# Optimization experiments

Measured on AMD Instinct MI355X. Metric: run time of the kernel, lower is better.

## Reference

```python
import jax, jax.numpy as jnp
import numpy as np

IN_CH, OUT_CH, HEAD, QK_DIM, V_DIM = 256, 256, 8, 512, 512


def setup_inputs() -> dict:
    key = jax.random.key(0)
    ks = jax.random.split(key, 5)
    B, H, W = 16, 32, 32
    x = jax.random.normal(ks[0], (B, IN_CH, H, W), dtype=jnp.float32)
    # 1x1 conv weights stored as [out_ch, in_ch]
    qkv_out = 2 * QK_DIM + V_DIM
    qkv_w = jax.random.normal(ks[1], (qkv_out, IN_CH), dtype=jnp.float32) * (IN_CH ** -0.5)
    qkv_b = jax.random.normal(ks[2], (qkv_out,), dtype=jnp.float32) * 0.02
    proj_w = jax.random.normal(ks[3], (OUT_CH, V_DIM), dtype=jnp.float32) * (V_DIM ** -0.5)
    proj_b = jax.random.normal(ks[4], (OUT_CH,), dtype=jnp.float32) * 0.02
    return {"x": x, "qkv_w": qkv_w, "qkv_b": qkv_b, "proj_w": proj_w, "proj_b": proj_b}


def reference(x, qkv_w, qkv_b, proj_w, proj_b):
    B, C, H, W = x.shape
    N = H * W
    dh = QK_DIM // HEAD
    dv = V_DIM // HEAD
    scale = dh ** -0.5
    # 1x1 conv == channel GEMM
    qkv = jnp.einsum('bchw,oc->bohw', x, qkv_w) + qkv_b[None, :, None, None]
    q, k, v = jnp.split(qkv, [QK_DIM, 2 * QK_DIM], axis=1)
    # [B, ch, H, W] -> [B, head, N, head_dim]
    def to_heads(t, d):
        return t.reshape(B, HEAD, d, N).transpose(0, 1, 3, 2)
    q = to_heads(q, dh)
    k = to_heads(k, dh)
    v = to_heads(v, dv)
    mask = jnp.tril(jnp.ones((N, N), dtype=bool))  # [N, N]
    scores = jnp.einsum('bhnd,bhmd->bhnm', q, k) * scale
    scores = jnp.where(mask, scores, -jnp.inf)
    attn = jax.nn.softmax(scores, axis=-1)
    attn = jnp.where(mask, attn, 0.0)
    out = jnp.einsum('bhnm,bhmd->bhnd', attn, v)  # [B, head, N, dv]
    out = out.transpose(0, 1, 3, 2).reshape(B, V_DIM, H, W)
    out = jnp.einsum('bvhw,ov->bohw', out, proj_w) + proj_b[None, :, None, None]
    return out
```

## Files before the change

kernel.cpp:

```cpp
#include <hip/hip_runtime.h>
#include <math.h>

static constexpr int Bsz = 16;
static constexpr int Np  = 1024;
static constexpr int Cin = 256;

typedef __attribute__((ext_vector_type(8))) short short8;
typedef __attribute__((ext_vector_type(4))) float f4;

#if defined(__has_builtin)
#if __has_builtin(__builtin_amdgcn_exp2f)
#define EXP2(x) __builtin_amdgcn_exp2f(x)
#else
#define EXP2(x) exp2f(x)
#endif
#else
#define EXP2(x) exp2f(x)
#endif

#define QSCALE 0.18033688011112f

__device__ __forceinline__ unsigned short f2b(float f) {
    union { float fp; unsigned int u; } v; v.fp = f;
    unsigned int r = v.u + 0x7fffu + ((v.u >> 16) & 1u);
    return (unsigned short)(r >> 16);
}

__global__ __launch_bounds__(256)
void cast_xw(const float* __restrict__ x, const float* __restrict__ qw,
             const float* __restrict__ pw, ushort* __restrict__ xb,
             ushort* __restrict__ qwb, ushort* __restrict__ pwb)
{
    const int t = threadIdx.x;
    if (blockIdx.y < 4) {
        __shared__ ushort T[64][72];
        const int n0 = blockIdx.x * 64, c0 = blockIdx.y * 64, b = blockIdx.z;
        {
            const int c_l = t >> 2, ns = (t & 3) * 16;
            const float* src = &x[((b * Cin + c0 + c_l) << 10) + n0 + ns];
#pragma unroll
            for (int i = 0; i < 4; ++i) {
                const float4 v = *(const float4*)(src + 4 * i);
                T[ns + 4 * i + 0][c_l] = f2b(v.x);
                T[ns + 4 * i + 1][c_l] = f2b(v.y);
                T[ns + 4 * i + 2][c_l] = f2b(v.z);
                T[ns + 4 * i + 3][c_l] = f2b(v.w);
            }
        }
        __syncthreads();
        {
            const int n_l = t >> 2, cs = (t & 3) * 16;
            ushort* dst = &xb[((b << 10) + n0 + n_l) * Cin + c0 + cs];
            *(uint4*)dst       = *(const uint4*)&T[n_l][cs];
            *(uint4*)(dst + 8) = *(const uint4*)&T[n_l][cs + 8];
        }
    } else {
        const int nq4 = (1536 * Cin) / 4;
        const int base = ((blockIdx.z * 16 + blockIdx.x) * 256 + t) * 2;
#pragma unroll
        for (int g = 0; g < 2; ++g) {
            const int j = base + g;
            const float* src; ushort* dst; int jj;
            if (j < nq4) { src = qw; dst = qwb; jj = j; }
            else         { src = pw; dst = pwb; jj = j - nq4; }
            const float4 v = *(const float4*)(src + 4 * jj);
            ushort4 u; u.x = f2b(v.x); u.y = f2b(v.y); u.z = f2b(v.z); u.w = f2b(v.w);
            *(ushort4*)(dst + 4 * jj) = u;
        }
    }
}

__global__ __launch_bounds__(256)
void qkv_gemm(const ushort* __restrict__ xb, const ushort* __restrict__ wb,
              const float* __restrict__ bias,
              ushort* __restrict__ qb, ushort* __restrict__ kb, ushort* __restrict__ vb)
{
    __shared__ ushort lds[18432];
    ushort* As = lds;
    ushort* Bs = lds + 9216;

    const int t = threadIdx.x;
    const int w = t >> 6, lane = t & 63, quad = lane >> 4, ln = lane & 15;
    const int n0 = blockIdx.x * 128;
    const int o0 = blockIdx.y * 128;
    const int b  = blockIdx.z;
    const int ow = (w & 1) * 64, nw = (w >> 1) * 64;
    const bool vpath = (o0 >= 1024);

    f4 acc[4][4];
#pragma unroll
    for (int i = 0; i < 4; ++i)
#pragma unroll
        for (int j = 0; j < 4; ++j) acc[i][j] = (f4){0.f, 0.f, 0.f, 0.f};

    const int rr = t >> 2, cc = (t & 3) * 16;
    for (int k0 = 0; k0 < Cin; k0 += 64) {
        __syncthreads();
#pragma unroll
        for (int p = 0; p < 2; ++p) {
            const int row = rr + p * 64;
            const ushort* sa = &wb[(o0 + row) * Cin + k0 + cc];
            *(uint4*)&As[row * 72 + cc]     = *(const uint4*)sa;
            *(uint4*)&As[row * 72 + cc + 8] = *(const uint4*)(sa + 8);
            const ushort* sb = &xb[((b << 10) + n0 + row) * Cin + k0 + cc];
            *(uint4*)&Bs[row * 72 + cc]     = *(const uint4*)sb;
            *(uint4*)&Bs[row * 72 + cc + 8] = *(const uint4*)(sb + 8);
        }
        __syncthreads();
#pragma unroll
        for (int sub = 0; sub < 2; ++sub) {
            short8 af[4], bf[4];
#pragma unroll
            for (int ot = 0; ot < 4; ++ot)
                af[ot] = *(const short8*)&As[(ow + ot * 16 + ln) * 72 + sub * 32 + quad * 8];
#pragma unroll
            for (int nt = 0; nt < 4; ++nt)
                bf[nt] = *(const short8*)&Bs[(nw + nt * 16 + ln) * 72 + sub * 32 + quad * 8];
            if (!vpath) {
#pragma unroll
                for (int ot = 0; ot < 4; ++ot)
#pragma unroll
                    for (int nt = 0; nt < 4; ++nt)
                        acc[ot][nt] = __builtin_amdgcn_mfma_f32_16x16x32_bf16(
                            af[ot], bf[nt], acc[ot][nt], 0, 0, 0);
            } else {
#pragma unroll
                for (int nt = 0; nt < 4; ++nt)
#pragma unroll
                    for (int ot = 0; ot < 4; ++ot)
                        acc[nt][ot] = __builtin_amdgcn_mfma_f32_16x16x32_bf16(
                            bf[nt], af[ot], acc[nt][ot], 0, 0, 0);
            }
        }
    }

    __syncthreads();
    if (!vpath) {
        ushort* Ct = lds;
        const float sc = (o0 < 512) ? QSCALE : 1.0f;
#pragma unroll
        for (int ot = 0; ot < 4; ++ot) {
            float bs[4];
#pragma unroll
            for (int rg = 0; rg < 4; ++rg)
                bs[rg] = bias[o0 + ow + ot * 16 + quad * 4 + rg];
#pragma unroll
            for (int nt = 0; nt < 4; ++nt) {
                ushort4 u;
                u.x = f2b((acc[ot][nt][0] + bs[0]) * sc);
                u.y = f2b((acc[ot][nt][1] + bs[1]) * sc);
                u.z = f2b((acc[ot][nt][2] + bs[2]) * sc);
                u.w = f2b((acc[ot][nt][3] + bs[3]) * sc);
                *(ushort4*)&Ct[(nw + nt * 16 + ln) * 136 + ow + ot * 16 + quad * 4] = u;
            }
        }
        __syncthreads();
        ushort* dst; int obase;
        if (o0 < 512) { dst = qb; obase = o0; }
        else          { dst = kb; obase = o0 - 512; }
        const int rn = t >> 1, hf = t & 1;
        const int bh = b * 8 + (obase >> 6) + hf;
        ushort* drow = &dst[(bh * Np + n0 + rn) << 6];
        const ushort* srow = &Ct[rn * 136 + hf * 64];
#pragma unroll
        for (int s = 0; s < 8; ++s)
            *(uint4*)(drow + s * 8) = *(const uint4*)(srow + s * 8);
    } else {
        ushort* Ct = lds;
#pragma unroll
        for (int ot = 0; ot < 4; ++ot) {
            const float bo = bias[o0 + ow + ot * 16 + ln];
#pragma unroll
            for (int nt = 0; nt < 4; ++nt) {
                ushort4 u;
                u.x = f2b(acc[nt][ot][0] + bo);
                u.y = f2b(acc[nt][ot][1] + bo);
                u.z = f2b(acc[nt][ot][2] + bo);
                u.w = f2b(acc[nt][ot][3] + bo);
                *(ushort4*)&Ct[(ow + ot * 16 + ln) * 136 + nw + nt * 16 + quad * 4] = u;
            }
        }
        __syncthreads();
        const int o_l = t >> 1, nh = (t & 1) * 64;
        const int bh = b * 8 + ((o0 - 1024) >> 6) + (o_l >> 6);
        ushort* drow = &vb[((size_t)bh << 16) + ((o_l & 63) << 10) + n0 + nh];
        const ushort* srow = &Ct[o_l * 136 + nh];
#pragma unroll
        for (int s = 0; s < 8; ++s)
            *(uint4*)(drow + s * 8) = *(const uint4*)(srow + s * 8);
    }
}

__global__ __launch_bounds__(256, 4)
void attn(const ushort* __restrict__ qb, const ushort* __restrict__ kb,
          const ushort* __restrict__ vt, ushort* __restrict__ ob)
{
    __shared__ ushort Qs[64 * 72];
    __shared__ ushort Ks[64 * 72];
    __shared__ ushort Vt[64 * 72];
    __shared__ ushort Ps[64 * 72];

    const int t    = threadIdx.x;
    const int w    = t >> 6;
    const int lane = t & 63;
    const int quad = lane >> 4;
    const int ln   = lane & 15;
    const int bh   = blockIdx.x & 127;
    const int qt   = 15 - (blockIdx.x >> 7);
    const int q0   = qt * 64;

    {
        const int r = t & 63, seg = t >> 6;
        const ushort* src = &qb[((bh * Np + q0 + r) << 6) + seg * 16];
        *(uint4*)&Qs[r * 72 + seg * 16]     = *(const uint4*)src;
        *(uint4*)&Qs[r * 72 + seg * 16 + 8] = *(const uint4*)(src + 8);
    }
    __syncthreads();

    const short8 qa0 = *(const short8*)&Qs[(w * 16 + ln) * 72 + quad * 8];
    const short8 qa1 = *(const short8*)&Qs[(w * 16 + ln) * 72 + 32 + quad * 8];

    f4 o_[4];
#pragma unroll
    for (int nt = 0; nt < 4; ++nt) o_[nt] = (f4){0.f, 0.f, 0.f, 0.f};
    float mrun = -INFINITY, lrun = 0.f;

    for (int kt = 0; kt <= qt; ++kt) {
        __syncthreads();
        {
            const int r = t & 63, seg = t >> 6;
            const ushort* sk = &kb[((bh * Np + kt * 64 + r) << 6) + seg * 16];
            *(uint4*)&Ks[r * 72 + seg * 16]     = *(const uint4*)sk;
            *(uint4*)&Ks[r * 72 + seg * 16 + 8] = *(const uint4*)(sk + 8);
            const int dd = t >> 2, c = (t & 3) * 16;
            const ushort* sv = &vt[((size_t)bh << 16) + (dd << 10) + kt * 64 + c];
            *(uint4*)&Vt[dd * 72 + c]     = *(const uint4*)sv;
            *(uint4*)&Vt[dd * 72 + c + 8] = *(const uint4*)(sv + 8);
        }
        __syncthreads();

        const bool diag = (kt == qt);

        f4 st[4];
#pragma unroll
        for (int mt = 0; mt < 4; ++mt) st[mt] = (f4){0.f, 0.f, 0.f, 0.f};
#pragma unroll
        for (int mt = 0; mt < 4; ++mt) {
            if (diag && mt > w) continue;
            const short8 ka0 = *(const short8*)&Ks[(mt * 16 + ln) * 72 + quad * 8];
            const short8 ka1 = *(const short8*)&Ks[(mt * 16 + ln) * 72 + 32 + quad * 8];
            st[mt] = __builtin_amdgcn_mfma_f32_16x16x32_bf16(ka0, qa0, st[mt], 0, 0, 0);
            st[mt] = __builtin_amdgcn_mfma_f32_16x16x32_bf16(ka1, qa1, st[mt], 0, 0, 0);
        }

        if (diag) {
            const int qrow = w * 16 + ln;
#pragma unroll
            for (int mt = 0; mt < 4; ++mt)
#pragma unroll
                for (int rg = 0; rg < 4; ++rg)
                    if (mt * 16 + quad * 4 + rg > qrow) st[mt][rg] = -INFINITY;
        }

        float mx = -INFINITY;
#pragma unroll
        for (int mt = 0; mt < 4; ++mt)
#pragma unroll
            for (int rg = 0; rg < 4; ++rg) mx = fmaxf(mx, st[mt][rg]);
        mx = fmaxf(mx, __shfl_xor(mx, 16));
        mx = fmaxf(mx, __shfl_xor(mx, 32));

        const float mn = fmaxf(mrun, mx);
        const float al = EXP2(mrun - mn);
        mrun = mn;

        float rs = 0.f;
        const int prow = (w * 16 + ln) * 72;
#pragma unroll
        for (int mt = 0; mt < 4; ++mt) {
            float p0 = EXP2(st[mt][0] - mn), p1 = EXP2(st[mt][1] - mn);
            float p2 = EXP2(st[mt][2] - mn), p3 = EXP2(st[mt][3] - mn);
            rs += (p0 + p1) + (p2 + p3);
            ushort4 u; u.x = f2b(p0); u.y = f2b(p1); u.z = f2b(p2); u.w = f2b(p3);
            *(ushort4*)&Ps[prow + mt * 16 + quad * 4] = u;
        }
        rs += __shfl_xor(rs, 16);
        rs += __shfl_xor(rs, 32);
        lrun = lrun * al + rs;

        float alr[4];
#pragma unroll
        for (int rg = 0; rg < 4; ++rg) alr[rg] = __shfl(al, quad * 4 + rg);
#pragma unroll
        for (int nt = 0; nt < 4; ++nt)
#pragma unroll
            for (int rg = 0; rg < 4; ++rg) o_[nt][rg] *= alr[rg];

#pragma unroll
        for (int ks = 0; ks < 2; ++ks) {
            if (diag && w * 16 + 15 < ks * 32) continue;
            const short8 pa = *(const short8*)&Ps[prow + ks * 32 + quad * 8];
#pragma unroll
            for (int nt = 0; nt < 4; ++nt) {
                const short8 vf = *(const short8*)&Vt[(nt * 16 + ln) * 72 + ks * 32 + quad * 8];
                o_[nt] = __builtin_amdgcn_mfma_f32_16x16x32_bf16(pa, vf, o_[nt], 0, 0, 0);
            }
        }
    }

    const float linv = 1.0f / lrun;
    float lr[4];
#pragma unroll
    for (int rg = 0; rg < 4; ++rg) lr[rg] = __shfl(linv, quad * 4 + rg);
#pragma unroll
    for (int rg = 0; rg < 4; ++rg) {
        const int rr = q0 + w * 16 + quad * 4 + rg;
#pragma unroll
        for (int nt = 0; nt < 4; ++nt)
            ob[((bh * Np + rr) << 6) + nt * 16 + ln] = f2b(o_[nt][rg] * lr[rg]);
    }
}

__global__ __launch_bounds__(256)
void proj_gemm(const ushort* __restrict__ obuf, const ushort* __restrict__ pwb,
               const float* __restrict__ bias, float* __restrict__ out)
{
    __shared__ ushort As[64 * 72];
    __shared__ ushort Bs[128 * 72];

    const int t = threadIdx.x;
    const int w = t >> 6, lane = t & 63, quad = lane >> 4, ln = lane & 15;
    const int n0 = blockIdx.x * 128;
    const int o0 = blockIdx.y * 64;
    const int b  = blockIdx.z;
    const int nw = w * 32;

    f4 acc[4][2];
#pragma unroll
    for (int i = 0; i < 4; ++i)
#pragma unroll
        for (int j = 0; j < 2; ++j) acc[i][j] = (f4){0.f, 0.f, 0.f, 0.f};

    const int rr = t >> 2, cc = (t & 3) * 16;
    for (int k0 = 0; k0 < 512; k0 += 64) {
        __syncthreads();
        {
            const ushort* sa = &pwb[(o0 + rr) * 512 + k0 + cc];
            *(uint4*)&As[rr * 72 + cc]     = *(const uint4*)sa;
            *(uint4*)&As[rr * 72 + cc + 8] = *(const uint4*)(sa + 8);
            const int head = k0 >> 6;
#pragma unroll
            for (int p = 0; p < 2; ++p) {
                const int row = rr + p * 64;
                const ushort* sb = &obuf[(((b * 8 + head) * Np + n0 + row) << 6) + cc];
                *(uint4*)&Bs[row * 72 + cc]     = *(const uint4*)sb;
                *(uint4*)&Bs[row * 72 + cc + 8] = *(const uint4*)(sb + 8);
            }
        }
        __syncthreads();
#pragma unroll
        for (int sub = 0; sub < 2; ++sub) {
            short8 af[4], bf[2];
#pragma unroll
            for (int ot = 0; ot < 4; ++ot)
                af[ot] = *(const short8*)&As[(ot * 16 + ln) * 72 + sub * 32 + quad * 8];
#pragma unroll
            for (int nt = 0; nt < 2; ++nt)
                bf[nt] = *(const short8*)&Bs[(nw + nt * 16 + ln) * 72 + sub * 32 + quad * 8];
#pragma unroll
            for (int ot = 0; ot < 4; ++ot)
#pragma unroll
                for (int nt = 0; nt < 2; ++nt)
                    acc[ot][nt] = __builtin_amdgcn_mfma_f32_16x16x32_bf16(
                        af[ot], bf[nt], acc[ot][nt], 0, 0, 0);
        }
    }

#pragma unroll
    for (int ot = 0; ot < 4; ++ot) {
#pragma unroll
        for (int rg = 0; rg < 4; ++rg) {
            const int oo = o0 + ot * 16 + quad * 4 + rg;
            const float pb = bias[oo];
            float* drow = &out[((b << 8) + oo) << 10];
#pragma unroll
            for (int nt = 0; nt < 2; ++nt)
                drow[n0 + nw + nt * 16 + ln] = acc[ot][nt][rg] + pb;
        }
    }
}

extern "C" void kernel_launch(void* const* d_in, const int* in_sizes, int n_in,
                              void* d_out, int out_size, void* d_ws, size_t ws_size,
                              hipStream_t stream)
{
    const float* x   = (const float*)d_in[0];
    const float* qw  = (const float*)d_in[1];
    const float* qbb = (const float*)d_in[2];
    const float* pw  = (const float*)d_in[3];
    const float* pb  = (const float*)d_in[4];
    float* out = (float*)d_out;

    const size_t per = (size_t)Bsz * 8 * Np * 64;
    ushort* qbuf = (ushort*)d_ws;
    ushort* kbuf = qbuf + per;
    ushort* vbuf = kbuf + per;
    ushort* obuf = vbuf + per;
    ushort* xb   = obuf + per;
    ushort* qwb  = xb + (size_t)Bsz * Np * Cin;
    ushort* pwb  = qwb + 1536 * Cin;

    cast_xw<<<dim3(16, 5, Bsz), 256, 0, stream>>>(x, qw, pw, xb, qwb, pwb);
    qkv_gemm<<<dim3(8, 12, Bsz), 256, 0, stream>>>(xb, qwb, qbb, qbuf, kbuf, vbuf);
    attn<<<dim3(128 * 16), 256, 0, stream>>>(qbuf, kbuf, vbuf, obuf);
    proj_gemm<<<dim3(8, 4, Bsz), 256, 0, stream>>>(obuf, pwb, pb, out);
}
```

Before: 164.8 us.

## Restructure attention so each wave owns 32 query rows and reads K/V from global

```diff
diff --git a/kernel.cpp b/kernel.cpp
--- a/kernel.cpp
+++ b/kernel.cpp
@@ -191,133 +191,146 @@
     }
 }
 
-__global__ __launch_bounds__(256, 4)
+__global__ __launch_bounds__(256)
 void attn(const ushort* __restrict__ qb, const ushort* __restrict__ kb,
           const ushort* __restrict__ vt, ushort* __restrict__ ob)
 {
-    __shared__ ushort Qs[64 * 72];
-    __shared__ ushort Ks[64 * 72];
-    __shared__ ushort Vt[64 * 72];
-    __shared__ ushort Ps[64 * 72];
-
-    const int t    = threadIdx.x;
-    const int w    = t >> 6;
-    const int lane = t & 63;
-    const int quad = lane >> 4;
-    const int ln   = lane & 15;
-    const int bh   = blockIdx.x & 127;
-    const int qt   = 15 - (blockIdx.x >> 7);
-    const int q0   = qt * 64;
-
-    {
-        const int r = t & 63, seg = t >> 6;
-        const ushort* src = &qb[((bh * Np + q0 + r) << 6) + seg * 16];
-        *(uint4*)&Qs[r * 72 + seg * 16]     = *(const uint4*)src;
-        *(uint4*)&Qs[r * 72 + seg * 16 + 8] = *(const uint4*)(src + 8);
-    }
-    __syncthreads();
-
-    const short8 qa0 = *(const short8*)&Qs[(w * 16 + ln) * 72 + quad * 8];
-    const short8 qa1 = *(const short8*)&Qs[(w * 16 + ln) * 72 + 32 + quad * 8];
-
-    f4 o_[4];
-#pragma unroll
-    for (int nt = 0; nt < 4; ++nt) o_[nt] = (f4){0.f, 0.f, 0.f, 0.f};
-    float mrun = -INFINITY, lrun = 0.f;
-
-    for (int kt = 0; kt <= qt; ++kt) {
-        __syncthreads();
-        {
-            const int r = t & 63, seg = t >> 6;
-            const ushort* sk = &kb[((bh * Np + kt * 64 + r) << 6) + seg * 16];
-            *(uint4*)&Ks[r * 72 + seg * 16]     = *(const uint4*)sk;
-            *(uint4*)&Ks[r * 72 + seg * 16 + 8] = *(const uint4*)(sk + 8);
-            const int dd = t >> 2, c = (t & 3) * 16;
-            const ushort* sv = &vt[((size_t)bh << 16) + (dd << 10) + kt * 64 + c];
-            *(uint4*)&Vt[dd * 72 + c]     = *(const uint4*)sv;
-            *(uint4*)&Vt[dd * 72 + c + 8] = *(const uint4*)(sv + 8);
-        }
-        __syncthreads();
-
-        const bool diag = (kt == qt);
-
-        f4 st[4];
-#pragma unroll
-        for (int mt = 0; mt < 4; ++mt) st[mt] = (f4){0.f, 0.f, 0.f, 0.f};
+    __shared__ ushort Ps[128 * 72];
+
+    const int t = threadIdx.x;
+    const int w = t >> 6, lane = t & 63, quad = lane >> 4, ln = lane & 15;
+    const int bh = blockIdx.x & 127;
+    const int qp = 7 - (blockIdx.x >> 7);
+    const int jj = qp * 4 + w;
+    const int q0 = jj * 32;
+    const int ktmax = (q0 + 31) >> 6;
+    const int pbase = (w * 32) * 72;
+
+    short8 qa[2][2];
+#pragma unroll
+    for (int s = 0; s < 2; ++s)
+#pragma unroll
+        for (int h = 0; h < 2; ++h)
+            qa[s][h] = *(const short8*)&qb[((bh * Np + q0 + s * 16 + ln) << 6) + h * 32 + quad * 8];
+
+    f4 ot[2][4];
+#pragma unroll
+    for (int s = 0; s < 2; ++s)
+#pragma unroll
+        for (int nt = 0; nt < 4; ++nt) ot[s][nt] = (f4){0.f, 0.f, 0.f, 0.f};
+    float mrun[2] = {-INFINITY, -INFINITY}, lrun[2] = {0.f, 0.f};
+
+    for (int kt = 0; kt <= ktmax; ++kt) {
+        const bool diag = (kt == ktmax);
+
+        f4 st[2][4];
 #pragma unroll
         for (int mt = 0; mt < 4; ++mt) {
-            if (diag && mt > w) continue;
-            const short8 ka0 = *(const short8*)&Ks[(mt * 16 + ln) * 72 + quad * 8];
-            const short8 ka1 = *(const short8*)&Ks[(mt * 16 + ln) * 72 + 32 + quad * 8];
-            st[mt] = __builtin_amdgcn_mfma_f32_16x16x32_bf16(ka0, qa0, st[mt], 0, 0, 0);
-            st[mt] = __builtin_amdgcn_mfma_f32_16x16x32_bf16(ka1, qa1, st[mt], 0, 0, 0);
+            const int kmin = kt * 64 + mt * 16;
+            if (diag && kmin > q0 + 31) {
+                st[0][mt] = (f4){-INFINITY, -INFINITY, -INFINITY, -INFINITY};
+                st[1][mt] = st[0][mt];
+                continue;
+            }
+            const ushort* krow = &kb[((bh * Np + kmin + ln) << 6) + quad * 8];
+            const short8 ka0 = *(const short8*)krow;
+            const short8 ka1 = *(const short8*)(krow + 32);
+#pragma unroll
+            for (int s = 0; s < 2; ++s) {
+                if (diag && kmin > q0 + s * 16 + 15) {
+                    st[s][mt] = (f4){-INFINITY, -INFINITY, -INFINITY, -INFINITY};
+                } else {
+                    f4 z = (f4){0.f, 0.f, 0.f, 0.f};
+                    z = __builtin_amdgcn_mfma_f32_16x16x32_bf16(ka0, qa[s][0], z, 0, 0, 0);
+                    st[s][mt] = __builtin_amdgcn_mfma_f32_16x16x32_bf16(ka1, qa[s][1], z, 0, 0, 0);
+                }
+            }
         }
 
         if (diag) {
-            const int qrow = w * 16 + ln;
+#pragma unroll
+            for (int s = 0; s < 2; ++s) {
+                const int q = q0 + s * 16 + ln;
+#pragma unroll
+                for (int mt = 0; mt < 4; ++mt) {
+                    const int kb_ = kt * 64 + mt * 16 + quad * 4;
+#pragma unroll
+                    for (int rg = 0; rg < 4; ++rg)
+                        if (kb_ + rg > q) st[s][mt][rg] = -INFINITY;
+                }
+            }
+        }
+
+#pragma unroll
+        for (int s = 0; s < 2; ++s) {
+            float mx = -INFINITY;
 #pragma unroll
             for (int mt = 0; mt < 4; ++mt)
 #pragma unroll
-                for (int rg = 0; rg < 4; ++rg)
-                    if (mt * 16 + quad * 4 + rg > qrow) st[mt][rg] = -INFINITY;
-        }
-
-        float mx = -INFINITY;
-#pragma unroll
-        for (int mt = 0; mt < 4; ++mt)
-#pragma unroll
-            for (int rg = 0; rg < 4; ++rg) mx = fmaxf(mx, st[mt][rg]);
-        mx = fmaxf(mx, __shfl_xor(mx, 16));
-        mx = fmaxf(mx, __shfl_xor(mx, 32));
-
-        const float mn = fmaxf(mrun, mx);
-        const float al = EXP2(mrun - mn);
-        mrun = mn;
-
-        float rs = 0.f;
-        const int prow = (w * 16 + ln) * 72;
-#pragma unroll
-        for (int mt = 0; mt < 4; ++mt) {
-            float p0 = EXP2(st[mt][0] - mn), p1 = EXP2(st[mt][1] - mn);
-            float p2 = EXP2(st[mt][2] - mn), p3 = EXP2(st[mt][3] - mn);
-            rs += (p0 + p1) + (p2 + p3);
-            ushort4 u; u.x = f2b(p0); u.y = f2b(p1); u.z = f2b(p2); u.w = f2b(p3);
-            *(ushort4*)&Ps[prow + mt * 16 + quad * 4] = u;
-        }
-        rs += __shfl_xor(rs, 16);
-        rs += __shfl_xor(rs, 32);
-        lrun = lrun * al + rs;
-
-        float alr[4];
-#pragma unroll
-        for (int rg = 0; rg < 4; ++rg) alr[rg] = __shfl(al, quad * 4 + rg);
-#pragma unroll
-        for (int nt = 0; nt < 4; ++nt)
-#pragma unroll
-            for (int rg = 0; rg < 4; ++rg) o_[nt][rg] *= alr[rg];
+                for (int rg = 0; rg < 4; ++rg) mx = fmaxf(mx, st[s][mt][rg]);
+            mx = fmaxf(mx, __shfl_xor(mx, 16));
+            mx = fmaxf(mx, __shfl_xor(mx, 32));
+
+            const float mn = fmaxf(mrun[s], mx);
+            const float al = EXP2(mrun[s] - mn);
+            mrun[s] = mn;
+
+            float rs = 0.f;
+            const int prow = pbase + (s * 16 + ln) * 72;
+#pragma unroll
+            for (int mt = 0; mt < 4; ++mt) {
+                const float p0 = EXP2(st[s][mt][0] - mn), p1 = EXP2(st[s][mt][1] - mn);
+                const float p2 = EXP2(st[s][mt][2] - mn), p3 = EXP2(st[s][mt][3] - mn);
+                rs += (p0 + p1) + (p2 + p3);
+                ushort4 u; u.x = f2b(p0); u.y = f2b(p1); u.z = f2b(p2); u.w = f2b(p3);
+                *(ushort4*)&Ps[prow + mt * 16 + quad * 4] = u;
+            }
+            rs += __shfl_xor(rs, 16);
+            rs += __shfl_xor(rs, 32);
+            lrun[s] = lrun[s] * al + rs;
+
+#pragma unroll
+            for (int nt = 0; nt < 4; ++nt)
+#pragma unroll
+                for (int rg = 0; rg < 4; ++rg) ot[s][nt][rg] *= al;
+        }
 
 #pragma unroll
         for (int ks = 0; ks < 2; ++ks) {
-            if (diag && w * 16 + 15 < ks * 32) continue;
-            const short8 pa = *(const short8*)&Ps[prow + ks * 32 + quad * 8];
+            const int kminh = kt * 64 + ks * 32;
+            if (diag && kminh > q0 + 31) continue;
+            const bool use0 = !diag || (kminh <= q0 + 15);
+            const short8 pa1 = *(const short8*)&Ps[pbase + (16 + ln) * 72 + ks * 32 + quad * 8];
+            short8 pa0;
+            if (use0) pa0 = *(const short8*)&Ps[pbase + (ln) * 72 + ks * 32 + quad * 8];
 #pragma unroll
             for (int nt = 0; nt < 4; ++nt) {
-                const short8 vf = *(const short8*)&Vt[(nt * 16 + ln) * 72 + ks * 32 + quad * 8];
-                o_[nt] = __builtin_amdgcn_mfma_f32_16x16x32_bf16(pa, vf, o_[nt], 0, 0, 0);
-            }
-        }
-    }
-
-    const float linv = 1.0f / lrun;
-    float lr[4];
-#pragma unroll
-    for (int rg = 0; rg < 4; ++rg) lr[rg] = __shfl(linv, quad * 4 + rg);
-#pragma unroll
-    for (int rg = 0; rg < 4; ++rg) {
-        const int rr = q0 + w * 16 + quad * 4 + rg;
-#pragma unroll
-        for (int nt = 0; nt < 4; ++nt)
-            ob[((bh * Np + rr) << 6) + nt * 16 + ln] = f2b(o_[nt][rg] * lr[rg]);
+                const short8 vf = *(const short8*)&vt[((size_t)bh << 16) +
+                    ((nt * 16 + ln) << 10) + kminh + quad * 8];
+                if (use0)
+                    ot[0][nt] = __builtin_amdgcn_mfma_f32_16x16x32_bf16(vf, pa0, ot[0][nt], 0, 0, 0);
+                ot[1][nt] = __builtin_amdgcn_mfma_f32_16x16x32_bf16(vf, pa1, ot[1][nt], 0, 0, 0);
+            }
+        }
+    }
+
+#pragma unroll
+    for (int s = 0; s < 2; ++s) {
+        const float linv = 1.0f / lrun[s];
+        const int prow = pbase + (s * 16 + ln) * 72;
+#pragma unroll
+        for (int nt = 0; nt < 4; ++nt) {
+            ushort4 u;
+            u.x = f2b(ot[s][nt][0] * linv);
+            u.y = f2b(ot[s][nt][1] * linv);
+            u.z = f2b(ot[s][nt][2] * linv);
+            u.w = f2b(ot[s][nt][3] * linv);
+            *(ushort4*)&Ps[prow + nt * 16 + quad * 4] = u;
+        }
+        const ushort* srow = &Ps[pbase + (s * 16 + ln) * 72 + quad * 16];
+        ushort* drow = &ob[((bh * Np + q0 + s * 16 + ln) << 6) + quad * 16];
+        *(uint4*)drow       = *(const uint4*)srow;
+        *(uint4*)(drow + 8) = *(const uint4*)(srow + 8);
     }
 }
 
@@ -412,6 +425,6 @@
 
     cast_xw<<<dim3(16, 5, Bsz), 256, 0, stream>>>(x, qw, pw, xb, qwb, pwb);
     qkv_gemm<<<dim3(8, 12, Bsz), 256, 0, stream>>>(xb, qwb, qbb, qbuf, kbuf, vbuf);
-    attn<<<dim3(128 * 16), 256, 0, stream>>>(qbuf, kbuf, vbuf, obuf);
+    attn<<<dim3(128 * 8), 256, 0, stream>>>(qbuf, kbuf, vbuf, obuf);
     proj_gemm<<<dim3(8, 4, Bsz), 256, 0, stream>>>(obuf, pwb, pb, out);
 }
```

New measurement: 198.6 us. 20.5% more time.
